# Performance work log

Measured on AMD Instinct MI355X. Metric: run time of the kernel, lower is better.

The kernel has to match this reference:

```python
import jax, jax.numpy as jnp
import numpy as np

D = 512
B = 8
N = 4096  # h = w = 64 grid


def _rmsnorm(x, eps=1e-6):
    # SimpleRMSNorm (no learned scale)
    return x * jax.lax.rsqrt(jnp.mean(jnp.square(x), axis=-1, keepdims=True) + eps)


def setup_inputs() -> dict:
    key = jax.random.key(0)
    ks = jax.random.split(key, 8)
    s = 1.0 / np.sqrt(D)
    return {
        "x": jax.random.normal(ks[0], (B, N, D), jnp.float32),
        "lower_bound": jax.random.uniform(ks[1], (1,), jnp.float32),
        "W_in": jax.random.normal(ks[2], (D, D), jnp.float32) * s,
        "b_in": jnp.zeros((D,), jnp.float32),
        "W_f": jax.random.normal(ks[3], (D, D), jnp.float32) * s,
        "b_f": jnp.zeros((D,), jnp.float32),
        "theta": jax.random.normal(ks[4], (D,), jnp.float32),
        "W_g": jax.random.normal(ks[5], (D, D), jnp.float32) * s,
        "b_g": jnp.zeros((D,), jnp.float32),
        "W_out": jax.random.normal(ks[6], (D, D), jnp.float32) * s,
        "b_out": jnp.zeros((D,), jnp.float32),
    }


def _gated_scan(decay, u, axis, reverse):
    # linear recurrence h_t = decay_t * h_{t-1} + u_t via associative scan
    def comb(e1, e2):
        a1, x1 = e1
        a2, x2 = e2
        return a1 * a2, a2 * x1 + x2
    _, y = jax.lax.associative_scan(comb, (decay, u), axis=axis, reverse=reverse)
    return y


def reference(x, lower_bound, W_in, b_in, W_f, b_f, theta, W_g, b_g, W_out, b_out):
    b, n, d = x.shape
    h = int(np.sqrt(n))
    w = n // h
    # b n d -> n b d -> h w b d
    xg = jnp.transpose(x, (1, 0, 2)).reshape(h, w, b, d)
    u = jax.nn.silu(xg @ W_in + b_in)              # candidate input
    f = jax.nn.sigmoid(xg @ W_f + b_f)             # forget gate
    lam = lower_bound + (1.0 - lower_bound) * f    # lower-bounded decay magnitude
    # complex decay lam * exp(i theta); complex input (1 - lam) * u
    decay = (lam * jnp.cos(theta) + 1j * (lam * jnp.sin(theta))).astype(jnp.complex64)
    inp = ((1.0 - lam) * u).astype(jnp.complex64)
    # bidirectional 2D scan: forward/backward over both grid axes (non-causal)
    hidden = jnp.zeros_like(u)
    for axis in (0, 1):
        for rev in (False, True):
            hidden = hidden + _gated_scan(decay, inp, axis, rev).real
    g = jax.nn.sigmoid(xg @ W_g + b_g)             # output gate
    y = (g * _rmsnorm(hidden)) @ W_out + b_out
    # h w b d -> n b d -> b n d
    return jnp.transpose(y.reshape(n, b, d), (1, 0, 2))
```

## Files before the change

### kernel.cpp

```cpp
#include <hip/hip_runtime.h>
#include <math.h>

#define DD 512
#define HG 64
#define M_ROWS 32768
#define ELEMS ((size_t)M_ROWS * DD)
#define LOG2E 1.44269504088896340736f

typedef __attribute__((ext_vector_type(8))) _Float16 f16x8;
typedef __attribute__((ext_vector_type(2))) _Float16 f16x2;
typedef __attribute__((ext_vector_type(4))) float f32x4;

__device__ __forceinline__ float fexp2_(float x) { return __builtin_amdgcn_exp2f(x); }
__device__ __forceinline__ float frcp_(float x)  { return __builtin_amdgcn_rcpf(x); }
__device__ __forceinline__ float fsig_(float v)  { return frcp_(1.0f + fexp2_(-v * LOG2E)); }

__global__ __launch_bounds__(256) void prep(
    const float* __restrict__ x, _Float16* __restrict__ x16,
    const float* __restrict__ W0, const float* __restrict__ W1,
    const float* __restrict__ W2, const float* __restrict__ W3,
    _Float16* __restrict__ WT)
{
    __shared__ float tile[64][65];
    if (blockIdx.x < 8192) {
        const size_t i = ((size_t)blockIdx.x * 256 + threadIdx.x) * 8;
        const float4 a = *(const float4*)&x[i];
        const float4 b = *(const float4*)&x[i + 4];
        f16x8 h;
        h[0] = (_Float16)a.x; h[1] = (_Float16)a.y;
        h[2] = (_Float16)a.z; h[3] = (_Float16)a.w;
        h[4] = (_Float16)b.x; h[5] = (_Float16)b.y;
        h[6] = (_Float16)b.z; h[7] = (_Float16)b.w;
        *(f16x8*)&x16[i] = h;
        return;
    }
    const int wb = blockIdx.x - 8192;
    const int z = wb >> 6;
    const int rem = wb & 63;
    const int n0 = (rem & 7) * 64, k0 = (rem >> 3) * 64;
    const float* W = (z == 0) ? W0 : (z == 1) ? W1 : (z == 2) ? W2 : W3;
    _Float16* dst = WT + (size_t)z * DD * DD;
    const int t = threadIdx.x;
    const int tr = t >> 6, tc = t & 63;
#pragma unroll
    for (int p = 0; p < 16; ++p)
        tile[p * 4 + tr][tc] = W[(size_t)(k0 + p * 4 + tr) * DD + n0 + tc];
    __syncthreads();
#pragma unroll
    for (int p = 0; p < 16; ++p) {
        const int nn = p * 4 + tr;
        dst[(size_t)(n0 + nn) * DD + k0 + tc] = (_Float16)tile[tc][nn];
    }
}

template <int MODE>
__global__ __launch_bounds__(256) void gemm_f16(
    const _Float16* __restrict__ A, const _Float16* __restrict__ WT,
    const float* __restrict__ b0, const float* __restrict__ b1,
    const float* __restrict__ b2, const float* __restrict__ lb_ptr,
    void* __restrict__ o0, void* __restrict__ o1, void* __restrict__ o2)
{
    __shared__ __align__(16) _Float16 As[2][128][32];
    __shared__ __align__(16) _Float16 Bs[2][128][32];

    const int NB = (MODE == 0) ? 12 : 4;
    const int lin = blockIdx.x;
    const int xcd = lin & 7;
    const int n_idx = (lin >> 3) % NB;
    const int mq = lin / (8 * NB);
    const int m0 = (xcd + 8 * mq) * 128;
    const int n0 = n_idx * 128;

    const int tid  = threadIdx.x;
    const int wave = tid >> 6;
    const int lane = tid & 63;
    const int wm = wave >> 1, wn = wave & 1;
    const int lrow = lane & 15;
    const int lk   = lane >> 4;

    const int srow  = lane >> 2;
    const int skoff = ((lane & 3) ^ ((lane >> 3) & 3)) * 8;
    const int ksw   = (lk ^ ((lrow >> 1) & 3)) * 8;

    f32x4 acc[4][4];
#pragma unroll
    for (int i = 0; i < 4; ++i)
#pragma unroll
        for (int j = 0; j < 4; ++j) acc[i][j] = (f32x4)(0.f);

    for (int k0 = 0; k0 < DD; k0 += 64) {
#pragma unroll
        for (int h = 0; h < 2; ++h) {
#pragma unroll
            for (int i = 0; i < 2; ++i) {
                const int row = wave * 32 + i * 16;
                const _Float16* bsrc =
                    WT + (size_t)(n0 + row + srow) * DD + k0 + h * 32 + skoff;
                __builtin_amdgcn_global_load_lds(
                    (const __attribute__((address_space(1))) void*)bsrc,
                    (__attribute__((address_space(3))) void*)&Bs[h][row][0], 16, 0, 0);
                const _Float16* asrc =
                    A + (size_t)(m0 + row + srow) * DD + k0 + h * 32 + skoff;
                __builtin_amdgcn_global_load_lds(
                    (const __attribute__((address_space(1))) void*)asrc,
                    (__attribute__((address_space(3))) void*)&As[h][row][0], 16, 0, 0);
            }
        }
        __syncthreads();
#pragma unroll
        for (int h = 0; h < 2; ++h) {
            f16x8 afr[4], bfr[4];
#pragma unroll
            for (int t = 0; t < 4; ++t) {
                afr[t] = *(const f16x8*)&As[h][wm * 64 + t * 16 + lrow][ksw];
                bfr[t] = *(const f16x8*)&Bs[h][wn * 64 + t * 16 + lrow][ksw];
            }
#pragma unroll
            for (int mt = 0; mt < 4; ++mt)
#pragma unroll
                for (int nt = 0; nt < 4; ++nt)
                    acc[mt][nt] = __builtin_amdgcn_mfma_f32_16x16x32_f16(
                        afr[mt], bfr[nt], acc[mt][nt], 0, 0, 0);
        }
        __syncthreads();
    }

    if (MODE == 0) {
        const int seg = n_idx >> 2;
        const float lbv = lb_ptr[0];
        const float* bias = (seg == 0) ? b0 : (seg == 1) ? b1 : b2;
        _Float16* outp = (seg == 0) ? (_Float16*)o0
                       : (seg == 1) ? (_Float16*)o1 : (_Float16*)o2;
        const int cb = (n_idx & 3) * 128 + wn * 64;
#pragma unroll
        for (int mt = 0; mt < 4; ++mt) {
#pragma unroll
            for (int nt = 0; nt < 4; ++nt) {
                const int col = cb + nt * 16 + lrow;
                const float bcol = bias[col];
#pragma unroll
                for (int r = 0; r < 4; ++r) {
                    const int row = m0 + wm * 64 + mt * 16 + lk * 4 + r;
                    const float v = acc[mt][nt][r] + bcol;
                    float res;
                    if (seg == 0)      res = (1.0f - lbv) * frcp_(1.0f + fexp2_(v * LOG2E));
                    else if (seg == 1) res = v * fsig_(v);
                    else               res = fsig_(v);
                    outp[(size_t)row * DD + col] = (_Float16)res;
                }
            }
        }
    } else {
        float* outp = (float*)o0;
#pragma unroll
        for (int mt = 0; mt < 4; ++mt) {
#pragma unroll
            for (int nt = 0; nt < 4; ++nt) {
                const int col = n0 + wn * 64 + nt * 16 + lrow;
                const float bcol = b0[col];
#pragma unroll
                for (int r = 0; r < 4; ++r) {
                    const int row = m0 + wm * 64 + mt * 16 + lk * 4 + r;
                    outp[(size_t)row * DD + col] = acc[mt][nt][r] + bcol;
                }
            }
        }
    }
}

__global__ __launch_bounds__(256) void scan2(
    const _Float16* __restrict__ dm, const _Float16* __restrict__ u,
    const float* __restrict__ theta,
    _Float16* __restrict__ ha, _Float16* __restrict__ hb)
{
    const int t = (blockIdx.x & 511) * 256 + threadIdx.x;
    const bool is_i = blockIdx.x >= 512;
    const int dp = t & 255;
    const int line = t >> 8;
    const int d0 = dp * 2;
    size_t base, stride;
    _Float16* hout;
    if (!is_i) {
        base = (size_t)line * (HG * DD) + d0; stride = DD; hout = ha;
    } else {
        const int bb = line >> 6, j = line & 63;
        base = (size_t)bb * (HG * HG * DD) + (size_t)j * DD + d0;
        stride = (size_t)HG * DD; hout = hb;
    }
    float s0, c0, s1, c1;
    sincosf(theta[d0], &s0, &c0);
    sincosf(theta[d0 + 1], &s1, &c1);

    f16x2 fr[HG];
    float yr0 = 0.f, yi0 = 0.f, yr1 = 0.f, yi1 = 0.f;
#pragma unroll
    for (int k = 0; k < HG; ++k) {
        const size_t idx = base + (size_t)k * stride;
        const f16x2 dp2 = *(const f16x2*)&dm[idx];
        const f16x2 up2 = *(const f16x2*)&u[idx];
        const float dm0 = (float)dp2[0], dm1 = (float)dp2[1];
        const float lm0 = 1.0f - dm0, lm1 = 1.0f - dm1;
        float nr = fmaf(lm0, c0 * yr0 - s0 * yi0, dm0 * (float)up2[0]);
        yi0 = lm0 * (c0 * yi0 + s0 * yr0); yr0 = nr;
        nr = fmaf(lm1, c1 * yr1 - s1 * yi1, dm1 * (float)up2[1]);
        yi1 = lm1 * (c1 * yi1 + s1 * yr1); yr1 = nr;
        f16x2 p; p[0] = (_Float16)yr0; p[1] = (_Float16)yr1;
        fr[k] = p;
    }
    yr0 = 0.f; yi0 = 0.f; yr1 = 0.f; yi1 = 0.f;
#pragma unroll
    for (int k = HG - 1; k >= 0; --k) {
        const size_t idx = base + (size_t)k * stride;
        const f16x2 dp2 = *(const f16x2*)&dm[idx];
        const f16x2 up2 = *(const f16x2*)&u[idx];
        const float dm0 = (float)dp2[0], dm1 = (float)dp2[1];
        const float lm0 = 1.0f - dm0, lm1 = 1.0f - dm1;
        float nr = fmaf(lm0, c0 * yr0 - s0 * yi0, dm0 * (float)up2[0]);
        yi0 = lm0 * (c0 * yi0 + s0 * yr0); yr0 = nr;
        nr = fmaf(lm1, c1 * yr1 - s1 * yi1, dm1 * (float)up2[1]);
        yi1 = lm1 * (c1 * yi1 + s1 * yr1); yr1 = nr;
        f16x2 o;
        o[0] = (_Float16)((float)fr[k][0] + yr0);
        o[1] = (_Float16)((float)fr[k][1] + yr1);
        *(f16x2*)&hout[idx] = o;
    }
}

__global__ __launch_bounds__(256) void gate_rmsnorm(
    const _Float16* __restrict__ ha, const _Float16* __restrict__ hb,
    const _Float16* __restrict__ g, _Float16* __restrict__ v)
{
    const int row = blockIdx.x;
    const int t = threadIdx.x;
    const size_t b0 = (size_t)row * DD + t * 2;
    const f16x2 a = *(const f16x2*)&ha[b0];
    const f16x2 b = *(const f16x2*)&hb[b0];
    const float h0 = (float)a[0] + (float)b[0];
    const float h1 = (float)a[1] + (float)b[1];
    float ss = h0 * h0 + h1 * h1;
#pragma unroll
    for (int off = 32; off > 0; off >>= 1) ss += __shfl_down(ss, off, 64);
    __shared__ float wsum[4];
    __shared__ float rms_s;
    if ((t & 63) == 0) wsum[t >> 6] = ss;
    __syncthreads();
    if (t == 0) {
        const float tot = wsum[0] + wsum[1] + wsum[2] + wsum[3];
        rms_s = rsqrtf(tot * (1.0f / (float)DD) + 1e-6f);
    }
    __syncthreads();
    const float rms = rms_s;
    const f16x2 gg = *(const f16x2*)&g[b0];
    f16x2 o;
    o[0] = (_Float16)((float)gg[0] * h0 * rms);
    o[1] = (_Float16)((float)gg[1] * h1 * rms);
    *(f16x2*)&v[b0] = o;
}

extern "C" void kernel_launch(void* const* d_in, const int* in_sizes, int n_in,
                              void* d_out, int out_size, void* d_ws, size_t ws_size,
                              hipStream_t stream)
{
    const float* x     = (const float*)d_in[0];
    const float* lb    = (const float*)d_in[1];
    const float* W_in  = (const float*)d_in[2];
    const float* b_in  = (const float*)d_in[3];
    const float* W_f   = (const float*)d_in[4];
    const float* b_f   = (const float*)d_in[5];
    const float* theta = (const float*)d_in[6];
    const float* W_g   = (const float*)d_in[7];
    const float* b_g   = (const float*)d_in[8];
    const float* W_out = (const float*)d_in[9];
    const float* b_out = (const float*)d_in[10];

    float* out = (float*)d_out;
    char* wsb  = (char*)d_ws;

    _Float16* dm_v = (_Float16*)wsb;
    _Float16* u_b  = (_Float16*)(wsb + ELEMS * 2);
    _Float16* g_b  = (_Float16*)(wsb + ELEMS * 4);
    _Float16* WT   = (_Float16*)(wsb + ELEMS * 6);
    const size_t WSEG = (size_t)DD * DD;

    _Float16* ha  = (_Float16*)d_out;
    _Float16* x16 = (_Float16*)((char*)d_out + ELEMS * 2);
    _Float16* hb  = x16;

    prep<<<8448, 256, 0, stream>>>(x, x16, W_f, W_in, W_g, W_out, WT);

    gemm_f16<0><<<3072, 256, 0, stream>>>(x16, WT, b_f, b_in, b_g, lb,
                                          dm_v, u_b, g_b);

    scan2<<<1024, 256, 0, stream>>>(dm_v, u_b, theta, ha, hb);

    gate_rmsnorm<<<M_ROWS, 256, 0, stream>>>(ha, hb, g_b, dm_v);

    gemm_f16<1><<<1024, 256, 0, stream>>>(dm_v, WT + 3 * WSEG, b_out, nullptr,
                                          nullptr, nullptr, out, nullptr, nullptr);
}
```

Measured before the change: 344.1 us.

## Split scan lines into four chunks with shared-memory carry combination

The 64-step bidirectional complex scan is split into 4 chunks of 16 steps per line, each handled by its own wavefront. Each chunk computes a local scan and its aggregate decay (product of magnitudes times a rotation by theta to the 16th power), exchanges these through shared memory, then rescans its chunk starting from the combined carry. This shortens the serial dependency chain and quadruples the number of threads, aiming for more latency hiding. The cost is a second pass of scan arithmetic, register-held input chunks, and a block-wide barrier.

```diff
diff --git a/kernel.cpp b/kernel.cpp
--- a/kernel.cpp
+++ b/kernel.cpp
@@ -168,16 +168,33 @@
     }
 }
 
-__global__ __launch_bounds__(256) void scan2(
+#define CH 4
+#define CL 16
+
+#define STEP(K, YR0, YI0, YR1, YI1) {                                      \
+    const float dm0_ = (float)dmr[K][0], dm1_ = (float)dmr[K][1];          \
+    const float lm0_ = 1.0f - dm0_, lm1_ = 1.0f - dm1_;                    \
+    float nr_ = fmaf(lm0_, c0 * (YR0) - s0 * (YI0), dm0_ * (float)ur[K][0]); \
+    YI0 = lm0_ * (c0 * (YI0) + s0 * (YR0)); YR0 = nr_;                     \
+    nr_ = fmaf(lm1_, c1 * (YR1) - s1 * (YI1), dm1_ * (float)ur[K][1]);     \
+    YI1 = lm1_ * (c1 * (YI1) + s1 * (YR1)); YR1 = nr_; }
+
+__global__ __launch_bounds__(256, 4) void scan2(
     const _Float16* __restrict__ dm, const _Float16* __restrict__ u,
     const float* __restrict__ theta,
     _Float16* __restrict__ ha, _Float16* __restrict__ hb)
 {
-    const int t = (blockIdx.x & 511) * 256 + threadIdx.x;
-    const bool is_i = blockIdx.x >= 512;
-    const int dp = t & 255;
-    const int line = t >> 8;
-    const int d0 = dp * 2;
+    __shared__ float ex[CH][64][13];
+
+    const int blk  = blockIdx.x & 2047;
+    const bool is_i = blockIdx.x >= 2048;
+    const int tid   = threadIdx.x;
+    const int chunk = tid >> 6;
+    const int dpl   = tid & 63;
+    const int dpg   = blk & 3;
+    const int line  = blk >> 2;
+    const int d0    = (dpg * 64 + dpl) * 2;
+
     size_t base, stride;
     _Float16* hout;
     if (!is_i) {
@@ -187,44 +204,93 @@
         base = (size_t)bb * (HG * HG * DD) + (size_t)j * DD + d0;
         stride = (size_t)HG * DD; hout = hb;
     }
+    const size_t cbase = base + (size_t)(chunk * CL) * stride;
+
     float s0, c0, s1, c1;
     sincosf(theta[d0], &s0, &c0);
     sincosf(theta[d0 + 1], &s1, &c1);
 
-    f16x2 fr[HG];
-    float yr0 = 0.f, yi0 = 0.f, yr1 = 0.f, yi1 = 0.f;
-#pragma unroll
-    for (int k = 0; k < HG; ++k) {
-        const size_t idx = base + (size_t)k * stride;
-        const f16x2 dp2 = *(const f16x2*)&dm[idx];
-        const f16x2 up2 = *(const f16x2*)&u[idx];
-        const float dm0 = (float)dp2[0], dm1 = (float)dp2[1];
-        const float lm0 = 1.0f - dm0, lm1 = 1.0f - dm1;
-        float nr = fmaf(lm0, c0 * yr0 - s0 * yi0, dm0 * (float)up2[0]);
-        yi0 = lm0 * (c0 * yi0 + s0 * yr0); yr0 = nr;
-        nr = fmaf(lm1, c1 * yr1 - s1 * yi1, dm1 * (float)up2[1]);
-        yi1 = lm1 * (c1 * yi1 + s1 * yr1); yr1 = nr;
+    f16x2 dmr[CL], ur[CL];
+#pragma unroll
+    for (int k = 0; k < CL; ++k) {
+        dmr[k] = *(const f16x2*)&dm[cbase + (size_t)k * stride];
+        ur[k]  = *(const f16x2*)&u [cbase + (size_t)k * stride];
+    }
+
+    float fr0 = 0.f, fi0 = 0.f, fr1 = 0.f, fi1 = 0.f;
+    float P0 = 1.f, P1 = 1.f;
+#pragma unroll
+    for (int k = 0; k < CL; ++k) {
+        const float dm0_ = (float)dmr[k][0], dm1_ = (float)dmr[k][1];
+        const float lm0_ = 1.0f - dm0_, lm1_ = 1.0f - dm1_;
+        P0 *= lm0_; P1 *= lm1_;
+        float nr_ = fmaf(lm0_, c0 * fr0 - s0 * fi0, dm0_ * (float)ur[k][0]);
+        fi0 = lm0_ * (c0 * fi0 + s0 * fr0); fr0 = nr_;
+        nr_ = fmaf(lm1_, c1 * fr1 - s1 * fi1, dm1_ * (float)ur[k][1]);
+        fi1 = lm1_ * (c1 * fi1 + s1 * fr1); fr1 = nr_;
+    }
+    float br0 = 0.f, bi0 = 0.f, br1 = 0.f, bi1 = 0.f;
+#pragma unroll
+    for (int k = CL - 1; k >= 0; --k) STEP(k, br0, bi0, br1, bi1);
+
+    float rc0 = c0, rs0 = s0, rc1 = c1, rs1 = s1;
+#pragma unroll
+    for (int q = 0; q < 4; ++q) {
+        float t0 = rc0 * rc0 - rs0 * rs0; rs0 = 2.f * rc0 * rs0; rc0 = t0;
+        float t1 = rc1 * rc1 - rs1 * rs1; rs1 = 2.f * rc1 * rs1; rc1 = t1;
+    }
+
+    {
+        float* e = ex[chunk][dpl];
+        e[0]  = P0 * rc0; e[1]  = P0 * rs0;
+        e[2]  = fr0;      e[3]  = fi0;
+        e[4]  = br0;      e[5]  = bi0;
+        e[6]  = P1 * rc1; e[7]  = P1 * rs1;
+        e[8]  = fr1;      e[9]  = fi1;
+        e[10] = br1;      e[11] = bi1;
+    }
+    __syncthreads();
+
+    float cfr0 = 0.f, cfi0 = 0.f, cfr1 = 0.f, cfi1 = 0.f;
+    for (int cc = 0; cc < chunk; ++cc) {
+        const float* e = ex[cc][dpl];
+        float nr = e[2] + e[0] * cfr0 - e[1] * cfi0;
+        cfi0     = e[3] + e[0] * cfi0 + e[1] * cfr0;
+        cfr0 = nr;
+        nr       = e[8] + e[6] * cfr1 - e[7] * cfi1;
+        cfi1     = e[9] + e[6] * cfi1 + e[7] * cfr1;
+        cfr1 = nr;
+    }
+    float cbr0 = 0.f, cbi0 = 0.f, cbr1 = 0.f, cbi1 = 0.f;
+    for (int cc = CH - 1; cc > chunk; --cc) {
+        const float* e = ex[cc][dpl];
+        float nr = e[4] + e[0] * cbr0 - e[1] * cbi0;
+        cbi0     = e[5] + e[0] * cbi0 + e[1] * cbr0;
+        cbr0 = nr;
+        nr       = e[10] + e[6] * cbr1 - e[7] * cbi1;
+        cbi1     = e[11] + e[6] * cbi1 + e[7] * cbr1;
+        cbr1 = nr;
+    }
+
+    float yr0 = cfr0, yi0 = cfi0, yr1 = cfr1, yi1 = cfi1;
+    f16x2 fres[CL];
+#pragma unroll
+    for (int k = 0; k < CL; ++k) {
+        STEP(k, yr0, yi0, yr1, yi1);
         f16x2 p; p[0] = (_Float16)yr0; p[1] = (_Float16)yr1;
-        fr[k] = p;
-    }
-    yr0 = 0.f; yi0 = 0.f; yr1 = 0.f; yi1 = 0.f;
-#pragma unroll
-    for (int k = HG - 1; k >= 0; --k) {
-        const size_t idx = base + (size_t)k * stride;
-        const f16x2 dp2 = *(const f16x2*)&dm[idx];
-        const f16x2 up2 = *(const f16x2*)&u[idx];
-        const float dm0 = (float)dp2[0], dm1 = (float)dp2[1];
-        const float lm0 = 1.0f - dm0, lm1 = 1.0f - dm1;
-        float nr = fmaf(lm0, c0 * yr0 - s0 * yi0, dm0 * (float)up2[0]);
-        yi0 = lm0 * (c0 * yi0 + s0 * yr0); yr0 = nr;
-        nr = fmaf(lm1, c1 * yr1 - s1 * yi1, dm1 * (float)up2[1]);
-        yi1 = lm1 * (c1 * yi1 + s1 * yr1); yr1 = nr;
+        fres[k] = p;
+    }
+    yr0 = cbr0; yi0 = cbi0; yr1 = cbr1; yi1 = cbi1;
+#pragma unroll
+    for (int k = CL - 1; k >= 0; --k) {
+        STEP(k, yr0, yi0, yr1, yi1);
         f16x2 o;
-        o[0] = (_Float16)((float)fr[k][0] + yr0);
-        o[1] = (_Float16)((float)fr[k][1] + yr1);
-        *(f16x2*)&hout[idx] = o;
-    }
-}
+        o[0] = (_Float16)((float)fres[k][0] + yr0);
+        o[1] = (_Float16)((float)fres[k][1] + yr1);
+        *(f16x2*)&hout[cbase + (size_t)k * stride] = o;
+    }
+}
+#undef STEP
 
 __global__ __launch_bounds__(256) void gate_rmsnorm(
     const _Float16* __restrict__ ha, const _Float16* __restrict__ hb,
@@ -291,7 +357,7 @@
     gemm_f16<0><<<3072, 256, 0, stream>>>(x16, WT, b_f, b_in, b_g, lb,
                                           dm_v, u_b, g_b);
 
-    scan2<<<1024, 256, 0, stream>>>(dm_v, u_b, theta, ha, hb);
+    scan2<<<4096, 256, 0, stream>>>(dm_v, u_b, theta, ha, hb);
 
     gate_rmsnorm<<<M_ROWS, 256, 0, stream>>>(ha, hb, g_b, dm_v);
 
```

After: 292.8 us. 14.9% less time.
